# Kernel optimization log

Measured on AMD Instinct MI355X. Metric: run time of the kernel, lower is better.

Reference implementation:

```python
import jax, jax.numpy as jnp
import numpy as np
from jax import lax

KSIZE, SIGMA, ALPHA = 9, 7.0, 0.05
DN = ('NCHW', 'OIHW', 'NCHW')

def _sobel_weights():
    sx = np.array([[-1, 0, 1], [-2, 0, 2], [-1, 0, 1]], np.float32)
    sy = np.array([[-1, -2, -1], [0, 0, 0], [1, 2, 1]], np.float32)
    return jnp.asarray(np.stack([sx, sy])[:, None])  # (2,1,3,3)

def _gauss_weights():
    ax = np.arange(KSIZE, dtype=np.float32) - (KSIZE - 1) / 2.0
    g1 = np.exp(-(ax ** 2) / (2.0 * SIGMA ** 2))
    g2 = np.outer(g1, g1)
    g2 = g2 / g2.sum()
    return jnp.asarray(g2[None, None])  # (1,1,9,9)

def setup_inputs() -> dict:
    key = jax.random.key(0)
    x = jax.random.normal(key, (1, 1, 4096, 4096), dtype=jnp.float32)
    return {"x": x, "sobel_w": _sobel_weights(), "gauss_w": _gauss_weights()}

def reference(x, sobel_w, gauss_w):
    # Image gradients (Sobel, zero padding, cross-correlation like torch Conv2d)
    g = lax.conv_general_dilated(x, sobel_w, (1, 1), [(1, 1), (1, 1)], dimension_numbers=DN)  # (N,2,H,W)
    Ix, Iy = g[:, 0:1], g[:, 1:2]
    # Channel products Ixx, Iyy, Ixy
    prods = jnp.concatenate([Ix * Ix, Iy * Iy, Ix * Iy], axis=1)  # (N,3,H,W)
    # Second moment: same Gaussian applied per channel (depthwise)
    gk = jnp.tile(gauss_w, (3, 1, 1, 1))  # (3,1,9,9)
    pad = (KSIZE - 1) // 2
    S = lax.conv_general_dilated(prods, gk, (1, 1), [(pad, pad), (pad, pad)],
                                 feature_group_count=3, dimension_numbers=DN)
    Sxx, Syy, Sxy = S[:, 0:1], S[:, 1:2], S[:, 2:3]
    # Corner response R = det - alpha*trace^2
    tr = Sxx + Syy
    R = Sxx * Syy - Sxy * Sxy - ALPHA * tr * tr  # (N,1,H,W)
    # NMS: threshold below median (torch.median = lower middle element), 7x7 maxpool, keep maxima
    med = jnp.quantile(R, 0.5, method='lower')
    Rt = jnp.where(R > med, R, jnp.zeros_like(R))
    pooled = lax.reduce_window(Rt, -jnp.inf, lax.max, (1, 1, 7, 7), (1, 1, 1, 1),
                               [(0, 0), (0, 0), (3, 3), (3, 3)])
    mask = jnp.where(Rt == pooled, jnp.ones_like(Rt), jnp.zeros_like(Rt))
    return mask * Rt
```

## Files before the change

kernel.cpp:

```cpp
#include <hip/hip_runtime.h>
#include <math.h>

#define HW 4096
#define NPIX (HW * HW)
#define N4 (NPIX / 4)
#define TS 32
#define MED_RANK 8388607u
#define NOBIN 0xFFFFFFFFu
#define H1_COPIES 16
#define H23_COPIES 4

typedef unsigned int u32;
typedef unsigned long long u64;

__device__ __forceinline__ u32 f2key(float f) {
  u32 u = __float_as_uint(f);
  return (u & 0x80000000u) ? ~u : (u | 0x80000000u);
}

__device__ __forceinline__ void wave_hist_add(u32* lh, u32 bin) {
  int lane = threadIdx.x & 63;
  u32 prev = __shfl_up(bin, 1);
  bool head = (lane == 0) || (prev != bin);
  u64 hb = __ballot(head);
  u64 after = (lane < 63) ? (hb >> (lane + 1)) : 0ull;
  int run = after ? __ffsll((long long)after) : (64 - lane);
  if (head && bin != NOBIN) atomicAdd(&lh[bin], (u32)run);
}

template <int RT, bool POOL>
__global__ __launch_bounds__(256, 4) void harris_main(
    const float* __restrict__ x, const float* __restrict__ gw,
    const u32* __restrict__ sel, float* __restrict__ Rout,
    u32* __restrict__ h1) {
  constexpr int PR = RT + 8;
  constexpr int XR = RT + 10;
  constexpr int CGR = (RT + 3) / 4;
  constexpr int VP = ((((CGR - 1) * 4 + 12) + 3) / 4) * 4 + 4;
  constexpr int RTD = POOL ? RT : 1;
  constexpr int NH = POOL ? 1 : 1024;
  constexpr int XIN_F = XR * (XR + 2);
  constexpr int V_F = 3 * RT * VP;
  constexpr int UNI_F = (XIN_F > V_F) ? XIN_F : V_F;

  __shared__ __align__(16) float uni[UNI_F];
  __shared__ float p0[PR][PR], p1[PR][PR], p2[PR][PR];
  __shared__ float g1s[12];
  __shared__ float rt[RTD][RTD + 2];
  __shared__ float hm[RTD][TS];
  __shared__ u32 lh[NH];

  float(*xin)[XR + 2] = (float(*)[XR + 2])uni;
  float(*v)[VP] = (float(*)[VP])uni;

  const int tid = threadIdx.x;
  const int or0 = blockIdx.y * TS - (POOL ? 3 : 0);
  const int oc0 = blockIdx.x * TS - (POOL ? 3 : 0);
  const int xr0 = or0 - 5, xc0 = oc0 - 5;

  if constexpr (!POOL)
    for (int i = tid; i < NH; i += 256) lh[i] = 0u;

  if (tid < 9) {
    float s = 0.f;
#pragma unroll
    for (int j = 0; j < 9; ++j) s += gw[tid * 9 + j];
    g1s[tid] = s;
  }

  for (int idx = tid; idx < XR * XR; idx += 256) {
    int r = idx / XR, c = idx % XR;
    int gr = xr0 + r, gc = xc0 + c;
    float val = 0.f;
    if ((u32)gr < (u32)HW && (u32)gc < (u32)HW) val = x[(size_t)gr * HW + gc];
    xin[r][c] = val;
  }
  __syncthreads();

  if constexpr (!POOL) {
    for (int task = tid; task < PR * (PR / 4); task += 256) {
      int r = task / (PR / 4);
      int c4 = (task % (PR / 4)) * 4;
      int gr = or0 - 4 + r;
      int gc0 = oc0 - 4 + c4;
      __align__(16) float a[3][8];
#pragma unroll
      for (int rr = 0; rr < 3; ++rr) {
        *(float4*)&a[rr][0] = *(const float4*)&xin[r + rr][c4];
        *(float4*)&a[rr][4] = *(const float4*)&xin[r + rr][c4 + 4];
      }
      float4 P0, P1, P2;
      float* p0v = (float*)&P0;
      float* p1v = (float*)&P1;
      float* p2v = (float*)&P2;
#pragma unroll
      for (int o = 0; o < 4; ++o) {
        float Ix = (a[0][o + 2] - a[0][o]) + 2.f * (a[1][o + 2] - a[1][o]) +
                   (a[2][o + 2] - a[2][o]);
        float Iy = (a[2][o] - a[0][o]) + 2.f * (a[2][o + 1] - a[0][o + 1]) +
                   (a[2][o + 2] - a[0][o + 2]);
        bool in = ((u32)gr < (u32)HW) && ((u32)(gc0 + o) < (u32)HW);
        p0v[o] = in ? Ix * Ix : 0.f;
        p1v[o] = in ? Iy * Iy : 0.f;
        p2v[o] = in ? Ix * Iy : 0.f;
      }
      *(float4*)&p0[r][c4] = P0;
      *(float4*)&p1[r][c4] = P1;
      *(float4*)&p2[r][c4] = P2;
    }
  } else {
    for (int idx = tid; idx < PR * PR; idx += 256) {
      int r = idx / PR, c = idx % PR;
      int gr = or0 - 4 + r, gc = oc0 - 4 + c;
      float P0 = 0.f, P1 = 0.f, P2 = 0.f;
      if ((u32)gr < (u32)HW && (u32)gc < (u32)HW) {
        float a00 = xin[r][c], a01 = xin[r][c + 1], a02 = xin[r][c + 2];
        float a10 = xin[r + 1][c], a12 = xin[r + 1][c + 2];
        float a20 = xin[r + 2][c], a21 = xin[r + 2][c + 1],
              a22 = xin[r + 2][c + 2];
        float Ix = (a02 - a00) + 2.f * (a12 - a10) + (a22 - a20);
        float Iy = (a20 - a00) + 2.f * (a21 - a01) + (a22 - a02);
        P0 = Ix * Ix;
        P1 = Iy * Iy;
        P2 = Ix * Iy;
      }
      p0[r][c] = P0;
      p1[r][c] = P1;
      p2[r][c] = P2;
    }
  }
  __syncthreads();

  float g[9];
#pragma unroll
  for (int k = 0; k < 9; ++k) g[k] = g1s[k];

  if constexpr (!POOL) {
    for (int task = tid; task < 3 * (RT / 8) * PR; task += 256) {
      int ch = task / ((RT / 8) * PR);
      int rem = task % ((RT / 8) * PR);
      int rg = (rem / PR) * 8;
      int c = rem % PR;
      const float(*pp)[PR] = (ch == 0) ? p0 : (ch == 1) ? p1 : p2;
      float col[16];
#pragma unroll
      for (int k = 0; k < 16; ++k) col[k] = pp[rg + k][c];
#pragma unroll
      for (int o = 0; o < 8; ++o) {
        float s = 0.f;
#pragma unroll
        for (int k = 0; k < 9; ++k) s = fmaf(g[k], col[o + k], s);
        v[ch * RT + rg + o][c] = s;
      }
    }
  } else {
    for (int task = tid; task < 3 * CGR * PR; task += 256) {
      int ch = task / (CGR * PR);
      int rem = task % (CGR * PR);
      int rg = (rem / PR) * 4;
      int c = rem % PR;
      const float(*pp)[PR] = (ch == 0) ? p0 : (ch == 1) ? p1 : p2;
      float col[12];
#pragma unroll
      for (int k = 0; k < 12; ++k) col[k] = (rg + k < PR) ? pp[rg + k][c] : 0.f;
#pragma unroll
      for (int o = 0; o < 4; ++o) {
        int rv = rg + o;
        if (rv < RT) {
          float s = 0.f;
#pragma unroll
          for (int k = 0; k < 9; ++k) s = fmaf(g[k], col[o + k], s);
          v[ch * RT + rv][c] = s;
        }
      }
    }
  }
  __syncthreads();

  float med = 0.f;
  if (POOL) med = __uint_as_float(sel[2]);

  for (int task = tid; task < RT * CGR; task += 256) {
    int r = task / CGR;
    int c0i = (task % CGR) * 4;
    float s3[3][4];
#pragma unroll
    for (int ch = 0; ch < 3; ++ch) {
      const float4* vp = (const float4*)&v[ch * RT + r][c0i];
      float4 w0 = vp[0], w1 = vp[1], w2 = vp[2];
      float row[12] = {w0.x, w0.y, w0.z, w0.w, w1.x, w1.y,
                       w1.z, w1.w, w2.x, w2.y, w2.z, w2.w};
#pragma unroll
      for (int o = 0; o < 4; ++o) {
        float s = 0.f;
#pragma unroll
        for (int k = 0; k < 9; ++k) s = fmaf(g[k], row[o + k], s);
        s3[ch][o] = s;
      }
    }
    if constexpr (!POOL) {
      float4 rv4;
      float* rp = (float*)&rv4;
#pragma unroll
      for (int o = 0; o < 4; ++o) {
        float Sxx = s3[0][o], Syy = s3[1][o], Sxy = s3[2][o];
        float tr = Sxx + Syy;
        rp[o] = Sxx * Syy - Sxy * Sxy - 0.05f * tr * tr;
      }
      *(float4*)&Rout[(size_t)(or0 + r) * HW + (oc0 + c0i)] = rv4;
#pragma unroll
      for (int o = 0; o < 4; ++o) wave_hist_add(lh, f2key(rp[o]) >> 22);
    } else {
#pragma unroll
      for (int o = 0; o < 4; ++o) {
        int c = c0i + o;
        if (c < RT) {
          float Sxx = s3[0][o], Syy = s3[1][o], Sxy = s3[2][o];
          float tr = Sxx + Syy;
          float Rv = Sxx * Syy - Sxy * Sxy - 0.05f * tr * tr;
          int gr = or0 + r, gc = oc0 + c;
          float val = -INFINITY;
          if ((u32)gr < (u32)HW && (u32)gc < (u32)HW)
            val = (Rv > med) ? Rv : 0.f;
          rt[r][c] = val;
        }
      }
    }
  }

  if constexpr (!POOL) {
    __syncthreads();
    const u32 cp = (u32)(blockIdx.y * gridDim.x + blockIdx.x) & (H1_COPIES - 1);
    u32* dst = h1 + cp * NH;
    for (int i = tid; i < NH; i += 256) {
      u32 c = lh[i];
      if (c) atomicAdd(&dst[i], c);
    }
  }

  if constexpr (POOL) {
    __syncthreads();
    for (int idx = tid; idx < RT * TS; idx += 256) {
      int r = idx / TS, c = idx % TS;
      float m = rt[r][c];
#pragma unroll
      for (int k = 1; k < 7; ++k) m = fmaxf(m, rt[r][c + k]);
      hm[r][c] = m;
    }
    __syncthreads();
    for (int idx = tid; idx < TS * TS; idx += 256) {
      int r = idx / TS, c = idx % TS;
      float pooled = hm[r][c];
#pragma unroll
      for (int k = 1; k < 7; ++k) pooled = fmaxf(pooled, hm[r + k][c]);
      float rc = rt[r + 3][c + 3];
      Rout[(size_t)(or0 + 3 + r) * HW + (oc0 + 3 + c)] =
          (rc == pooled) ? rc : 0.f;
    }
  }
}

__global__ __launch_bounds__(256) void hist_pass2(
    const float4* __restrict__ R4, const u32* __restrict__ sel,
    u32* __restrict__ hist) {
  __shared__ u32 lh[4096];
  for (int i = threadIdx.x; i < 4096; i += 256) lh[i] = 0u;
  const u32 p10 = sel[1] >> 22;
  __syncthreads();
  const u32 stride = gridDim.x * 256;
  for (u32 i = blockIdx.x * 256 + threadIdx.x; i < N4; i += stride) {
    float4 f = R4[i];
    const float* fp = (const float*)&f;
#pragma unroll
    for (int j = 0; j < 4; ++j) {
      u32 k = f2key(fp[j]);
      wave_hist_add(lh, ((k >> 22) == p10) ? ((k >> 10) & 0xFFFu) : NOBIN);
    }
  }
  __syncthreads();
  u32* dst = hist + (blockIdx.x & (H23_COPIES - 1)) * 4096;
  for (int i = threadIdx.x; i < 4096; i += 256) {
    u32 c = lh[i];
    if (c) atomicAdd(&dst[i], c);
  }
}

__global__ __launch_bounds__(256) void hist_pass3(
    const float4* __restrict__ R4, const u32* __restrict__ sel,
    u32* __restrict__ hist) {
  __shared__ u32 lh[1024];
  for (int i = threadIdx.x; i < 1024; i += 256) lh[i] = 0u;
  const u32 p22 = sel[1] >> 10;
  __syncthreads();
  const u32 stride = gridDim.x * 256;
  for (u32 i = blockIdx.x * 256 + threadIdx.x; i < N4; i += stride) {
    float4 f = R4[i];
    const float* fp = (const float*)&f;
#pragma unroll
    for (int j = 0; j < 4; ++j) {
      u32 k = f2key(fp[j]);
      if ((k >> 10) == p22) atomicAdd(&lh[k & 0x3FFu], 1u);
    }
  }
  __syncthreads();
  u32* dst = hist + (blockIdx.x & (H23_COPIES - 1)) * 1024;
  for (int i = threadIdx.x; i < 1024; i += 256) {
    u32 c = lh[i];
    if (c) atomicAdd(&dst[i], c);
  }
}

template <int NBINS, int NCOPY, int SHIFT, bool FIRST, bool LAST>
__global__ __launch_bounds__(256) void scan_select(const u32* __restrict__ hist,
                                                   u32* __restrict__ sel) {
  __shared__ u32 part[256];
  constexpr int C = NBINS / 256;
  int tid = threadIdx.x;
  u32 s = 0;
  for (int i = 0; i < C; ++i) {
    u32 b = 0;
#pragma unroll
    for (int cp = 0; cp < NCOPY; ++cp) b += hist[cp * NBINS + tid * C + i];
    s += b;
  }
  part[tid] = s;
  __syncthreads();
  if (tid == 0) {
    u32 r = FIRST ? MED_RANK : sel[0];
    u32 cum = 0;
    int seg = 0;
    for (; seg < 255; ++seg) {
      u32 ps = part[seg];
      if (cum + ps > r) break;
      cum += ps;
    }
    int b = seg * C;
    for (int i = 0; i < C; ++i) {
      u32 h = 0;
#pragma unroll
      for (int cp = 0; cp < NCOPY; ++cp) h += hist[cp * NBINS + b];
      if (cum + h > r) break;
      cum += h;
      ++b;
    }
    sel[0] = r - cum;
    u32 pfx = (FIRST ? 0u : sel[1]) | ((u32)b << SHIFT);
    sel[1] = pfx;
    if (LAST)
      sel[2] = (pfx & 0x80000000u) ? (pfx ^ 0x80000000u) : ~pfx;
  }
}

__global__ __launch_bounds__(256) void final_pool(const float* __restrict__ R,
                                                  const u32* __restrict__ sel,
                                                  float* __restrict__ out) {
  __shared__ __align__(16) float rt[38][44];
  __shared__ float hm[38][32];
  const float med = __uint_as_float(sel[2]);
  const int r0 = blockIdx.y * TS - 3;
  const int c0 = blockIdx.x * TS;
  const int c0m4 = c0 - 4;
  for (int idx = threadIdx.x; idx < 38 * 10; idx += 256) {
    int r = idx / 10, j = idx % 10;
    int gr = r0 + r, gc = c0m4 + 4 * j;
    float4 v4;
    float* vp = (float*)&v4;
    if ((u32)gr < (u32)HW && gc >= 0 && gc + 3 < HW) {
      float4 Rv = *(const float4*)&R[(size_t)gr * HW + gc];
      v4.x = (Rv.x > med) ? Rv.x : 0.f;
      v4.y = (Rv.y > med) ? Rv.y : 0.f;
      v4.z = (Rv.z > med) ? Rv.z : 0.f;
      v4.w = (Rv.w > med) ? Rv.w : 0.f;
    } else {
#pragma unroll
      for (int t = 0; t < 4; ++t) {
        int g2 = gc + t;
        float val = -INFINITY;
        if ((u32)gr < (u32)HW && (u32)g2 < (u32)HW) {
          float Rv = R[(size_t)gr * HW + g2];
          val = (Rv > med) ? Rv : 0.f;
        }
        vp[t] = val;
      }
    }
    *(float4*)&rt[r][4 * j] = v4;
  }
  __syncthreads();
  for (int idx = threadIdx.x; idx < 38 * TS; idx += 256) {
    int r = idx / TS, c = idx % TS;
    float m = rt[r][c + 1];
#pragma unroll
    for (int k = 2; k < 8; ++k) m = fmaxf(m, rt[r][c + k]);
    hm[r][c] = m;
  }
  __syncthreads();
  for (int idx = threadIdx.x; idx < TS * TS; idx += 256) {
    int r = idx / TS, c = idx % TS;
    float pooled = hm[r][c];
#pragma unroll
    for (int k = 1; k < 7; ++k) pooled = fmaxf(pooled, hm[r + k][c]);
    float rc = rt[r + 3][c + 4];
    out[(size_t)(r0 + 3 + r) * HW + (c0 + c)] = (rc == pooled) ? rc : 0.f;
  }
}

extern "C" void kernel_launch(void* const* d_in, const int* in_sizes, int n_in,
                              void* d_out, int out_size, void* d_ws,
                              size_t ws_size, hipStream_t stream) {
  (void)in_sizes;
  (void)n_in;
  (void)out_size;
  const float* x = (const float*)d_in[0];
  const float* gw = (const float*)d_in[2];
  float* out = (float*)d_out;

  const size_t RB = (size_t)NPIX * sizeof(float);
  const size_t HN = H1_COPIES * 1024 + H23_COPIES * 4096 + H23_COPIES * 1024 + 8;
  const size_t HB = HN * sizeof(u32);
  const bool planA = ws_size >= RB + HB;

  float* Rbuf;
  u32* hb;
  if (planA) {
    Rbuf = (float*)d_ws;
    hb = (u32*)((char*)d_ws + RB);
  } else {
    Rbuf = out;
    hb = (u32*)d_ws;
  }
  u32* h1 = hb;
  u32* h2 = h1 + H1_COPIES * 1024;
  u32* h3 = h2 + H23_COPIES * 4096;
  u32* sel = h3 + H23_COPIES * 1024;

  dim3 grid(HW / TS, HW / TS);
  hipMemsetAsync(hb, 0, HB, stream);
  harris_main<32, false><<<grid, 256, 0, stream>>>(x, gw, nullptr, Rbuf, h1);
  scan_select<1024, H1_COPIES, 22, true, false><<<1, 256, 0, stream>>>(h1, sel);
  hist_pass2<<<1024, 256, 0, stream>>>((const float4*)Rbuf, sel, h2);
  scan_select<4096, H23_COPIES, 10, false, false><<<1, 256, 0, stream>>>(h2, sel);
  hist_pass3<<<1024, 256, 0, stream>>>((const float4*)Rbuf, sel, h3);
  scan_select<1024, H23_COPIES, 0, false, true><<<1, 256, 0, stream>>>(h3, sel);
  if (planA) {
    final_pool<<<grid, 256, 0, stream>>>(Rbuf, sel, out);
  } else {
    harris_main<38, true><<<grid, 256, 0, stream>>>(x, gw, sel, out, nullptr);
  }
}
```

Measured before the change: 308.0 us.

## Add interior fast paths, vectorize vertical Gaussian, skip empty waves in histogram

Tiles that lie fully inside the image now load input and compute Sobel products without per-pixel bounds checks. The vertical Gaussian pass in the non-pool kernel is remapped so each of 240 threads produces a 4x4 block using float4 shared-memory loads and stores, replacing the scalar 8-row column tasks. The second histogram pass skips its wave-level histogram update whenever no lane in the wave has a key matching the selected prefix. Together these cut branch overhead, shared-memory instruction count and atomic/shuffle work, at the cost of more code paths and 16 idle threads in the vertical pass.

```diff
diff --git a/kernel.cpp b/kernel.cpp
--- a/kernel.cpp
+++ b/kernel.cpp
@@ -57,6 +57,8 @@
   const int or0 = blockIdx.y * TS - (POOL ? 3 : 0);
   const int oc0 = blockIdx.x * TS - (POOL ? 3 : 0);
   const int xr0 = or0 - 5, xc0 = oc0 - 5;
+  const bool inter =
+      (xr0 >= 0) && (xc0 >= 0) && (xr0 + XR <= HW) && (xc0 + XR <= HW);
 
   if constexpr (!POOL)
     for (int i = tid; i < NH; i += 256) lh[i] = 0u;
@@ -68,12 +70,19 @@
     g1s[tid] = s;
   }
 
-  for (int idx = tid; idx < XR * XR; idx += 256) {
-    int r = idx / XR, c = idx % XR;
-    int gr = xr0 + r, gc = xc0 + c;
-    float val = 0.f;
-    if ((u32)gr < (u32)HW && (u32)gc < (u32)HW) val = x[(size_t)gr * HW + gc];
-    xin[r][c] = val;
+  if (inter) {
+    for (int idx = tid; idx < XR * XR; idx += 256) {
+      int r = idx / XR, c = idx % XR;
+      xin[r][c] = x[(size_t)(xr0 + r) * HW + (xc0 + c)];
+    }
+  } else {
+    for (int idx = tid; idx < XR * XR; idx += 256) {
+      int r = idx / XR, c = idx % XR;
+      int gr = xr0 + r, gc = xc0 + c;
+      float val = 0.f;
+      if ((u32)gr < (u32)HW && (u32)gc < (u32)HW) val = x[(size_t)gr * HW + gc];
+      xin[r][c] = val;
+    }
   }
   __syncthreads();
 
@@ -81,8 +90,6 @@
     for (int task = tid; task < PR * (PR / 4); task += 256) {
       int r = task / (PR / 4);
       int c4 = (task % (PR / 4)) * 4;
-      int gr = or0 - 4 + r;
-      int gc0 = oc0 - 4 + c4;
       __align__(16) float a[3][8];
 #pragma unroll
       for (int rr = 0; rr < 3; ++rr) {
@@ -93,16 +100,31 @@
       float* p0v = (float*)&P0;
       float* p1v = (float*)&P1;
       float* p2v = (float*)&P2;
-#pragma unroll
-      for (int o = 0; o < 4; ++o) {
-        float Ix = (a[0][o + 2] - a[0][o]) + 2.f * (a[1][o + 2] - a[1][o]) +
-                   (a[2][o + 2] - a[2][o]);
-        float Iy = (a[2][o] - a[0][o]) + 2.f * (a[2][o + 1] - a[0][o + 1]) +
-                   (a[2][o + 2] - a[0][o + 2]);
-        bool in = ((u32)gr < (u32)HW) && ((u32)(gc0 + o) < (u32)HW);
-        p0v[o] = in ? Ix * Ix : 0.f;
-        p1v[o] = in ? Iy * Iy : 0.f;
-        p2v[o] = in ? Ix * Iy : 0.f;
+      if (inter) {
+#pragma unroll
+        for (int o = 0; o < 4; ++o) {
+          float Ix = (a[0][o + 2] - a[0][o]) + 2.f * (a[1][o + 2] - a[1][o]) +
+                     (a[2][o + 2] - a[2][o]);
+          float Iy = (a[2][o] - a[0][o]) + 2.f * (a[2][o + 1] - a[0][o + 1]) +
+                     (a[2][o + 2] - a[0][o + 2]);
+          p0v[o] = Ix * Ix;
+          p1v[o] = Iy * Iy;
+          p2v[o] = Ix * Iy;
+        }
+      } else {
+        int gr = or0 - 4 + r;
+        int gc0 = oc0 - 4 + c4;
+#pragma unroll
+        for (int o = 0; o < 4; ++o) {
+          float Ix = (a[0][o + 2] - a[0][o]) + 2.f * (a[1][o + 2] - a[1][o]) +
+                     (a[2][o + 2] - a[2][o]);
+          float Iy = (a[2][o] - a[0][o]) + 2.f * (a[2][o + 1] - a[0][o + 1]) +
+                     (a[2][o + 2] - a[0][o + 2]);
+          bool in = ((u32)gr < (u32)HW) && ((u32)(gc0 + o) < (u32)HW);
+          p0v[o] = in ? Ix * Ix : 0.f;
+          p1v[o] = in ? Iy * Iy : 0.f;
+          p2v[o] = in ? Ix * Iy : 0.f;
+        }
       }
       *(float4*)&p0[r][c4] = P0;
       *(float4*)&p1[r][c4] = P1;
@@ -136,21 +158,27 @@
   for (int k = 0; k < 9; ++k) g[k] = g1s[k];
 
   if constexpr (!POOL) {
-    for (int task = tid; task < 3 * (RT / 8) * PR; task += 256) {
-      int ch = task / ((RT / 8) * PR);
-      int rem = task % ((RT / 8) * PR);
-      int rg = (rem / PR) * 8;
-      int c = rem % PR;
+    if (tid < 240) {
+      int ch = tid / 80;
+      int rem = tid - ch * 80;
+      int rg = (rem / 10) * 4;
+      int c4 = (rem % 10) * 4;
       const float(*pp)[PR] = (ch == 0) ? p0 : (ch == 1) ? p1 : p2;
-      float col[16];
-#pragma unroll
-      for (int k = 0; k < 16; ++k) col[k] = pp[rg + k][c];
-#pragma unroll
-      for (int o = 0; o < 8; ++o) {
-        float s = 0.f;
-#pragma unroll
-        for (int k = 0; k < 9; ++k) s = fmaf(g[k], col[o + k], s);
-        v[ch * RT + rg + o][c] = s;
+      float4 col[12];
+#pragma unroll
+      for (int k = 0; k < 12; ++k) col[k] = *(const float4*)&pp[rg + k][c4];
+#pragma unroll
+      for (int o = 0; o < 4; ++o) {
+        float4 s = {0.f, 0.f, 0.f, 0.f};
+#pragma unroll
+        for (int k = 0; k < 9; ++k) {
+          float4 cv = col[o + k];
+          s.x = fmaf(g[k], cv.x, s.x);
+          s.y = fmaf(g[k], cv.y, s.y);
+          s.z = fmaf(g[k], cv.z, s.z);
+          s.w = fmaf(g[k], cv.w, s.w);
+        }
+        *(float4*)&v[ch * RT + rg + o][c4] = s;
       }
     }
   } else {
@@ -271,10 +299,17 @@
   for (u32 i = blockIdx.x * 256 + threadIdx.x; i < N4; i += stride) {
     float4 f = R4[i];
     const float* fp = (const float*)&f;
+    u32 k[4];
+    bool mt[4];
 #pragma unroll
     for (int j = 0; j < 4; ++j) {
-      u32 k = f2key(fp[j]);
-      wave_hist_add(lh, ((k >> 22) == p10) ? ((k >> 10) & 0xFFFu) : NOBIN);
+      k[j] = f2key(fp[j]);
+      mt[j] = (k[j] >> 22) == p10;
+    }
+    if (__ballot(mt[0] || mt[1] || mt[2] || mt[3])) {
+#pragma unroll
+      for (int j = 0; j < 4; ++j)
+        wave_hist_add(lh, mt[j] ? ((k[j] >> 10) & 0xFFFu) : NOBIN);
     }
   }
   __syncthreads();
@@ -438,7 +473,8 @@
   harris_main<32, false><<<grid, 256, 0, stream>>>(x, gw, nullptr, Rbuf, h1);
   scan_select<1024, H1_COPIES, 22, true, false><<<1, 256, 0, stream>>>(h1, sel);
   hist_pass2<<<1024, 256, 0, stream>>>((const float4*)Rbuf, sel, h2);
-  scan_select<4096, H23_COPIES, 10, false, false><<<1, 256, 0, stream>>>(h2, sel);
+  scan_select<4096, H23_COPIES, 10, false, false><<<1, 256, 0, stream>>>(h2,
+                                                                         sel);
   hist_pass3<<<1024, 256, 0, stream>>>((const float4*)Rbuf, sel, h3);
   scan_select<1024, H23_COPIES, 0, false, true><<<1, 256, 0, stream>>>(h3, sel);
   if (planA) {
```

After: 309.4 us. Within noise of the previous version (+0.5%).
